# Performance work log

Hardware: AMD Instinct MI355X
Metric: run time of the kernel (lower is better)

## Reference

```python
import jax, jax.numpy as jnp
import numpy as np
from jax import lax

V, E, H, B, T = 50000, 100, 64, 128, 1024


def setup_inputs() -> dict:
    key = jax.random.key(0)
    ks = jax.random.split(key, 16)
    def u(k, shape, fan):
        s = 1.0 / np.sqrt(fan)
        return jax.random.uniform(k, shape, jnp.float32, -s, s)
    x = jax.random.randint(ks[0], (B, T), 0, V)
    emb = jax.random.normal(ks[1], (V, E), jnp.float32)
    emb = emb.at[0].set(0.0)  # padding_idx=0
    return {
        'x': x,
        'emb': emb,
        'Wih0': u(ks[2], (4 * H, E), H), 'Whh0': u(ks[3], (4 * H, H), H),
        'bih0': u(ks[4], (4 * H,), H), 'bhh0': u(ks[5], (4 * H,), H),
        'Wih1': u(ks[6], (4 * H, H), H), 'Whh1': u(ks[7], (4 * H, H), H),
        'bih1': u(ks[8], (4 * H,), H), 'bhh1': u(ks[9], (4 * H,), H),
        'W1': u(ks[10], (H, H), H), 'b1': u(ks[11], (H,), H),
        'W2': u(ks[12], (1, H), H), 'b2': u(ks[13], (1,), H),
    }


def lstm_layer(inp, Wih, Whh, bih, bhh):
    # inp: [B, T, D]; PyTorch gate order i, f, g, o
    b, h = inp.shape[0], Whh.shape[1]
    xw = jnp.einsum('btd,gd->btg', inp, Wih) + bih + bhh  # [B, T, 4H]
    def step(carry, xw_t):
        hs, cs = carry
        gates = xw_t + hs @ Whh.T
        i, f, g, o = jnp.split(gates, 4, axis=-1)
        cs = jax.nn.sigmoid(f) * cs + jax.nn.sigmoid(i) * jnp.tanh(g)
        hs = jax.nn.sigmoid(o) * jnp.tanh(cs)
        return (hs, cs), hs
    init = (jnp.zeros((b, h), inp.dtype), jnp.zeros((b, h), inp.dtype))
    _, out = lax.scan(step, init, jnp.swapaxes(xw, 0, 1))  # [T, B, H]
    return jnp.swapaxes(out, 0, 1)


def reference(x, emb, Wih0, Whh0, bih0, bhh0, Wih1, Whh1, bih1, bhh1, W1, b1, W2, b2):
    e = emb[x]                                  # [B, T, E]
    h0 = lstm_layer(e, Wih0, Whh0, bih0, bhh0)  # [B, T, H]
    h1 = lstm_layer(h0, Wih1, Whh1, bih1, bhh1) # [B, T, H]
    last = h1[:, -1, :]                         # [B, H]
    z = jax.nn.relu(last @ W1.T + b1)           # dropout is identity in eval
    return jax.nn.sigmoid(z @ W2.T + b2)        # [B, 1]
```

## Files before the change

### kernel.cpp

```cpp
#include <hip/hip_runtime.h>
#include <hip/hip_bf16.h>

#define EMB_D 100
#define HID 64
#define G4 256
#define BATCH 128
#define SEQ 1024
#define TOK 64
#define LOG2E 1.44269504f

typedef _Float16 half2v __attribute__((ext_vector_type(2)));
typedef unsigned short u16;
typedef unsigned int   u32;

__device__ __forceinline__ float rcpf(float x) { return __builtin_amdgcn_rcpf(x); }
__device__ __forceinline__ float ex2(float x) { return __builtin_amdgcn_exp2f(x); }
__device__ __forceinline__ float sig_pre(float xp) { return rcpf(1.0f + ex2(-xp)); }
__device__ __forceinline__ float tanh_pre(float xp) {
  float t = ex2(-2.0f * fabsf(xp));
  return copysignf((1.0f - t) * rcpf(1.0f + t), xp);
}
__device__ __forceinline__ float tanh_nat(float x) {
  float t = ex2(-2.885390082f * fabsf(x));
  return copysignf((1.0f - t) * rcpf(1.0f + t), x);
}
__device__ __forceinline__ float sig_nat(float x) { return rcpf(1.0f + ex2(-LOG2E * x)); }

__device__ __forceinline__ float dot2(u32 h, u32 w, float acc) {
  return __builtin_amdgcn_fdot2(__builtin_bit_cast(half2v, h),
                                __builtin_bit_cast(half2v, w), acc, false);
}
__device__ __forceinline__ u32 packh2(float lo, float hi) {
  u16 a = __builtin_bit_cast(u16, (_Float16)lo);
  u16 b = __builtin_bit_cast(u16, (_Float16)hi);
  return (u32)a | ((u32)b << 16);
}
#define QP_XOR1 0xB1
#define QP_XOR2 0x4E
#define QP_XOR3 0x1B
#define QPERM(x, ctrl)                                                        \
  __builtin_bit_cast(float, __builtin_amdgcn_mov_dpp(                         \
      __builtin_bit_cast(int, (x)), (ctrl), 0xF, 0xF, true))

__global__ void prep_kernel(const float* __restrict__ Wih0,
                            const float* __restrict__ Whh0, const float* __restrict__ Wih1,
                            const float* __restrict__ Whh1,
                            const float* __restrict__ bih0, const float* __restrict__ bhh0,
                            const float* __restrict__ bih1, const float* __restrict__ bhh1,
                            u32* __restrict__ Wih0T2, float* __restrict__ b0c,
                            float* __restrict__ b1c,
                            u32* __restrict__ Whh0h, u32* __restrict__ Wih1h,
                            u32* __restrict__ Whh1h) {
  int g = threadIdx.x;
  b0c[g] = (bih0[g] + bhh0[g]) * LOG2E;
  b1c[g] = (bih1[g] + bhh1[g]) * LOG2E;
  for (int dp = 0; dp < 50; ++dp)
    Wih0T2[dp * G4 + g] = packh2(Wih0[g * EMB_D + 2 * dp] * LOG2E,
                                 Wih0[g * EMB_D + 2 * dp + 1] * LOG2E);
  for (int d = 0; d < 32; ++d) {
    Whh0h[g * 32 + d] = packh2(Whh0[g * HID + 2 * d] * LOG2E, Whh0[g * HID + 2 * d + 1] * LOG2E);
    Wih1h[g * 32 + d] = packh2(Wih1[g * HID + 2 * d] * LOG2E, Wih1[g * HID + 2 * d + 1] * LOG2E);
    Whh1h[g * 32 + d] = packh2(Whh1[g * HID + 2 * d] * LOG2E, Whh1[g * HID + 2 * d + 1] * LOG2E);
  }
}

__global__ __attribute__((amdgpu_waves_per_eu(1, 4))) __launch_bounds__(256)
void xw0_kernel(
    const int* __restrict__ x, const float* __restrict__ emb,
    const u32* __restrict__ Wih0T2, const float* __restrict__ b0c,
    _Float16* __restrict__ xw0h) {
  __shared__ int sidx[TOK];
  __shared__ alignas(16) u32 erow[TOK][52];
  int g = threadIdx.x;
  long t0 = (long)blockIdx.x * TOK;

  if (g < TOK) sidx[g] = x[t0 + g];
  __syncthreads();
  for (int i = g; i < TOK * 50; i += 256) {
    int tok = i / 50, dp = i - tok * 50;
    const float* er = emb + (size_t)sidx[tok] * EMB_D + 2 * dp;
    erow[tok][dp] = packh2(er[0], er[1]);
  }
  for (int i = g; i < TOK * 2; i += 256) erow[i >> 1][50 + (i & 1)] = 0;

  u32 wreg[52];
  #pragma unroll
  for (int dp = 0; dp < 50; ++dp) wreg[dp] = Wih0T2[dp * G4 + g];
  wreg[50] = 0; wreg[51] = 0;
  float bb = b0c[g];
  __syncthreads();

  for (int tok = 0; tok < TOK; ++tok) {
    const uint4* ep = (const uint4*)erow[tok];
    float a0 = bb, a1 = 0.f, a2 = 0.f, a3 = 0.f;
    #pragma unroll
    for (int c = 0; c < 13; ++c) {
      uint4 hv = ep[c];
      a0 = dot2(hv.x, wreg[4 * c],     a0);
      a1 = dot2(hv.y, wreg[4 * c + 1], a1);
      a2 = dot2(hv.z, wreg[4 * c + 2], a2);
      a3 = dot2(hv.w, wreg[4 * c + 3], a3);
    }
    xw0h[(t0 + tok) * G4 + g] = (_Float16)((a0 + a1) + (a2 + a3));
  }
}

__global__ __attribute__((amdgpu_waves_per_eu(1, 1))) __launch_bounds__(256)
void lstm_fused_kernel(
    const _Float16* __restrict__ xw0h,
    const u32* __restrict__ Whh0h, const u32* __restrict__ Wih1h,
    const u32* __restrict__ Whh1h, const float* __restrict__ b1c,
    const float* __restrict__ W1, const float* __restrict__ clsb1,
    const float* __restrict__ W2, const float* __restrict__ clsb2,
    float* __restrict__ out) {
  int tid = threadIdx.x;
  int l = tid & 63;
  int w = tid >> 6;
  int e = w * 16 + (l >> 2);
  int k = l & 3;
  int row = k * HID + e;
  int b = blockIdx.x;

  __shared__ alignas(16) _Float16 h0s[2][HID];
  __shared__ alignas(16) _Float16 h1s[2][HID];
  __shared__ alignas(16) float hf[HID];

  uint4 w0[8], w1[8], w2[8];
  {
    const uint4* p0 = (const uint4*)(Whh0h + row * 32);
    const uint4* p1 = (const uint4*)(Wih1h + row * 32);
    const uint4* p2 = (const uint4*)(Whh1h + row * 32);
    #pragma unroll
    for (int c = 0; c < 8; ++c) { w0[c] = p0[c]; w1[c] = p1[c]; w2[c] = p2[c]; }
  }
  #pragma unroll
  for (int c = 0; c < 8; ++c) {
    asm volatile("" : "+v"(w0[c].x), "+v"(w0[c].y), "+v"(w0[c].z), "+v"(w0[c].w));
    asm volatile("" : "+v"(w1[c].x), "+v"(w1[c].y), "+v"(w1[c].z), "+v"(w1[c].w));
    asm volatile("" : "+v"(w2[c].x), "+v"(w2[c].y), "+v"(w2[c].z), "+v"(w2[c].w));
  }
  float bias = b1c[row];

  if (tid < 128) ((u16*)h0s)[tid] = 0;
  else           ((u16*)h1s)[tid - 128] = 0;

  const _Float16* xr = xw0h + (long)b * SEQ * G4 + row;
  float xw_t = (float)xr[0];
  float xw_t1 = (float)xr[G4];
  float c0 = 0.f, c1 = 0.f;
  __syncthreads();

  for (int t = 0; t <= SEQ; ++t) {
    int rb = (t + 1) & 1, wb = t & 1;
    uint4 hc0[8], hc1[8];
    {
      const uint4* p0 = (const uint4*)h0s[rb];
      const uint4* p1 = (const uint4*)h1s[rb];
      #pragma unroll
      for (int c = 0; c < 8; ++c) { hc0[c] = p0[c]; hc1[c] = p1[c]; }
    }
    int tn = (t + 2 < SEQ) ? (t + 2) : (SEQ - 1);
    float xw_t2 = (float)xr[(long)tn * G4];

    if (t < SEQ) {
      float a0 = xw_t, a1 = 0.f, a2 = 0.f, a3 = 0.f;
      #pragma unroll
      for (int c = 0; c < 8; ++c) {
        a0 = dot2(hc0[c].x, w0[c].x, a0);
        a1 = dot2(hc0[c].y, w0[c].y, a1);
        a2 = dot2(hc0[c].z, w0[c].z, a2);
        a3 = dot2(hc0[c].w, w0[c].w, a3);
      }
      float g0 = (a0 + a1) + (a2 + a3);
      float g0x1 = QPERM(g0, QP_XOR1);
      float g0x2 = QPERM(g0, QP_XOR2);
      float g0x3 = QPERM(g0, QP_XOR3);
      c0 = sig_pre(g0x1) * c0 + sig_pre(g0) * tanh_pre(g0x2);
      float hv0 = sig_pre(g0x3) * tanh_nat(c0);
      if (k == 0) h0s[wb][e] = (_Float16)hv0;
    }

    if (t >= 1) {
      float a0 = bias, a1 = 0.f, a2 = 0.f, a3 = 0.f;
      float b0 = 0.f, b1 = 0.f, b2 = 0.f, b3 = 0.f;
      #pragma unroll
      for (int c = 0; c < 8; ++c) {
        a0 = dot2(hc0[c].x, w1[c].x, a0);
        a1 = dot2(hc0[c].y, w1[c].y, a1);
        a2 = dot2(hc0[c].z, w1[c].z, a2);
        a3 = dot2(hc0[c].w, w1[c].w, a3);
        b0 = dot2(hc1[c].x, w2[c].x, b0);
        b1 = dot2(hc1[c].y, w2[c].y, b1);
        b2 = dot2(hc1[c].z, w2[c].z, b2);
        b3 = dot2(hc1[c].w, w2[c].w, b3);
      }
      float g1 = ((a0 + a1) + (a2 + a3)) + ((b0 + b1) + (b2 + b3));
      float g1x1 = QPERM(g1, QP_XOR1);
      float g1x2 = QPERM(g1, QP_XOR2);
      float g1x3 = QPERM(g1, QP_XOR3);
      c1 = sig_pre(g1x1) * c1 + sig_pre(g1) * tanh_pre(g1x2);
      float hv1 = sig_pre(g1x3) * tanh_nat(c1);
      if (k == 0) {
        h1s[wb][e] = (_Float16)hv1;
        if (t == SEQ) hf[e] = hv1;
      }
    }

    xw_t = xw_t1; xw_t1 = xw_t2;
    asm volatile("s_waitcnt lgkmcnt(0)" ::: "memory");
    __builtin_amdgcn_s_barrier();
    asm volatile("" ::: "memory");
  }
  __syncthreads();

  if (w == 0) {
    int j = l;
    const float4* wp = (const float4*)(W1 + j * HID);
    const float4* hp = (const float4*)hf;
    float z0 = clsb1[j], z1 = 0.f, z2 = 0.f, z3 = 0.f;
    #pragma unroll
    for (int c = 0; c < 16; ++c) {
      float4 wv = wp[c];
      float4 hv = hp[c];
      z0 = fmaf(hv.x, wv.x, z0);
      z1 = fmaf(hv.y, wv.y, z1);
      z2 = fmaf(hv.z, wv.z, z2);
      z3 = fmaf(hv.w, wv.w, z3);
    }
    float z = fmaxf((z0 + z1) + (z2 + z3), 0.f);
    float v = z * W2[j];
    v += __shfl_xor(v, 1);
    v += __shfl_xor(v, 2);
    v += __shfl_xor(v, 4);
    v += __shfl_xor(v, 8);
    v += __shfl_xor(v, 16);
    v += __shfl_xor(v, 32);
    if (l == 0) out[b] = sig_nat(v + clsb2[0]);
  }
}

extern "C" void kernel_launch(void* const* d_in, const int* in_sizes, int n_in,
                              void* d_out, int out_size, void* d_ws, size_t ws_size,
                              hipStream_t stream) {
  const int*   x    = (const int*)d_in[0];
  const float* emb  = (const float*)d_in[1];
  const float* Wih0 = (const float*)d_in[2];
  const float* Whh0 = (const float*)d_in[3];
  const float* bih0 = (const float*)d_in[4];
  const float* bhh0 = (const float*)d_in[5];
  const float* Wih1 = (const float*)d_in[6];
  const float* Whh1 = (const float*)d_in[7];
  const float* bih1 = (const float*)d_in[8];
  const float* bhh1 = (const float*)d_in[9];
  const float* W1   = (const float*)d_in[10];
  const float* b1   = (const float*)d_in[11];
  const float* W2   = (const float*)d_in[12];
  const float* b2   = (const float*)d_in[13];
  float* out = (float*)d_out;

  char* ws = (char*)d_ws;
  const size_t XW0_BYTES = (size_t)BATCH * SEQ * G4 * sizeof(_Float16);
  _Float16* xw0h = (_Float16*)ws;     ws += XW0_BYTES;
  u32* Wih0T2    = (u32*)ws;          ws += (size_t)50 * G4 * sizeof(u32);
  float* b0c     = (float*)ws;        ws += G4 * sizeof(float);
  float* b1c     = (float*)ws;        ws += G4 * sizeof(float);
  u32* Whh0h     = (u32*)ws;          ws += (size_t)G4 * 32 * sizeof(u32);
  u32* Wih1h     = (u32*)ws;          ws += (size_t)G4 * 32 * sizeof(u32);
  u32* Whh1h     = (u32*)ws;          ws += (size_t)G4 * 32 * sizeof(u32);

  prep_kernel<<<1, 256, 0, stream>>>(Wih0, Whh0, Wih1, Whh1, bih0, bhh0, bih1, bhh1,
                                     Wih0T2, b0c, b1c, Whh0h, Wih1h, Whh1h);
  xw0_kernel<<<(BATCH * SEQ) / TOK, 256, 0, stream>>>(x, emb, Wih0T2, b0c, xw0h);
  lstm_fused_kernel<<<BATCH, 256, 0, stream>>>(xw0h, Whh0h, Wih1h, Whh1h, b1c,
                                               W1, b1, W2, b2, out);
}
```

Before: 737.6 us.

## Split hidden dot products across quad lanes with DPP reduction instead of gate split

Each quad of lanes previously owned one gate row each and computed the full 64-long dot product, then exchanged gate values via DPP. Now each lane computes a quarter of the K dimension for all four gates of a hidden unit, and the partial sums are reduced across the quad with two DPP adds. The xw0 precompute is rewritten in a gate-interleaved layout so each lane reads all four gate inputs with one 8-byte load. This shortens the per-step LDS read of h (32 bytes per lane instead of 128) and the serial dot2 chain, at the cost of extra DPP reduction steps and a lane-redundant activation computation.

```diff
diff --git a/kernel.cpp b/kernel.cpp
--- a/kernel.cpp
+++ b/kernel.cpp
@@ -35,12 +35,24 @@
   u16 b = __builtin_bit_cast(u16, (_Float16)hi);
   return (u32)a | ((u32)b << 16);
 }
-#define QP_XOR1 0xB1
-#define QP_XOR2 0x4E
-#define QP_XOR3 0x1B
-#define QPERM(x, ctrl)                                                        \
-  __builtin_bit_cast(float, __builtin_amdgcn_mov_dpp(                         \
-      __builtin_bit_cast(int, (x)), (ctrl), 0xF, 0xF, true))
+template <int CTRL>
+__device__ __forceinline__ float dppadd(float v) {
+  int x = __builtin_amdgcn_mov_dpp(__builtin_bit_cast(int, v), CTRL, 0xF, 0xF, true);
+  return v + __builtin_bit_cast(float, x);
+}
+#define QREDUCE(v) do { v = dppadd<0xB1>(v); v = dppadd<0x4E>(v); } while (0)
+
+__device__ __forceinline__ float q8(uint4 ha, uint4 hb, uint4 wa, uint4 wb) {
+  float a0 = dot2(ha.x, wa.x, 0.f);
+  float a1 = dot2(ha.y, wa.y, 0.f);
+  float a2 = dot2(ha.z, wa.z, 0.f);
+  float a3 = dot2(ha.w, wa.w, 0.f);
+  a0 = dot2(hb.x, wb.x, a0);
+  a1 = dot2(hb.y, wb.y, a1);
+  a2 = dot2(hb.z, wb.z, a2);
+  a3 = dot2(hb.w, wb.w, a3);
+  return (a0 + a1) + (a2 + a3);
+}
 
 __global__ void prep_kernel(const float* __restrict__ Wih0,
                             const float* __restrict__ Whh0, const float* __restrict__ Wih1,
@@ -48,12 +60,17 @@
                             const float* __restrict__ bih0, const float* __restrict__ bhh0,
                             const float* __restrict__ bih1, const float* __restrict__ bhh1,
                             u32* __restrict__ Wih0T2, float* __restrict__ b0c,
-                            float* __restrict__ b1c,
+                            float4* __restrict__ b1q,
                             u32* __restrict__ Whh0h, u32* __restrict__ Wih1h,
                             u32* __restrict__ Whh1h) {
   int g = threadIdx.x;
   b0c[g] = (bih0[g] + bhh0[g]) * LOG2E;
-  b1c[g] = (bih1[g] + bhh1[g]) * LOG2E;
+  if (g < HID) {
+    b1q[g] = make_float4((bih1[g] + bhh1[g]) * LOG2E,
+                         (bih1[g + 64] + bhh1[g + 64]) * LOG2E,
+                         (bih1[g + 128] + bhh1[g + 128]) * LOG2E,
+                         (bih1[g + 192] + bhh1[g + 192]) * LOG2E);
+  }
   for (int dp = 0; dp < 50; ++dp)
     Wih0T2[dp * G4 + g] = packh2(Wih0[g * EMB_D + 2 * dp] * LOG2E,
                                  Wih0[g * EMB_D + 2 * dp + 1] * LOG2E);
@@ -68,7 +85,7 @@
 void xw0_kernel(
     const int* __restrict__ x, const float* __restrict__ emb,
     const u32* __restrict__ Wih0T2, const float* __restrict__ b0c,
-    _Float16* __restrict__ xw0h) {
+    u16* __restrict__ xwP) {
   __shared__ int sidx[TOK];
   __shared__ alignas(16) u32 erow[TOK][52];
   int g = threadIdx.x;
@@ -90,6 +107,7 @@
   float bb = b0c[g];
   __syncthreads();
 
+  const int e = g & 63, q = g >> 6;
   for (int tok = 0; tok < TOK; ++tok) {
     const uint4* ep = (const uint4*)erow[tok];
     float a0 = bb, a1 = 0.f, a2 = 0.f, a3 = 0.f;
@@ -101,15 +119,16 @@
       a2 = dot2(hv.z, wreg[4 * c + 2], a2);
       a3 = dot2(hv.w, wreg[4 * c + 3], a3);
     }
-    xw0h[(t0 + tok) * G4 + g] = (_Float16)((a0 + a1) + (a2 + a3));
+    xwP[((size_t)(t0 + tok)) * G4 + e * 4 + q] =
+        __builtin_bit_cast(u16, (_Float16)((a0 + a1) + (a2 + a3)));
   }
 }
 
 __global__ __attribute__((amdgpu_waves_per_eu(1, 1))) __launch_bounds__(256)
 void lstm_fused_kernel(
-    const _Float16* __restrict__ xw0h,
+    const u16* __restrict__ xwP,
     const u32* __restrict__ Whh0h, const u32* __restrict__ Wih1h,
-    const u32* __restrict__ Whh1h, const float* __restrict__ b1c,
+    const u32* __restrict__ Whh1h, const float4* __restrict__ b1q,
     const float* __restrict__ W1, const float* __restrict__ clsb1,
     const float* __restrict__ W2, const float* __restrict__ clsb2,
     float* __restrict__ out) {
@@ -118,7 +137,6 @@
   int w = tid >> 6;
   int e = w * 16 + (l >> 2);
   int k = l & 3;
-  int row = k * HID + e;
   int b = blockIdx.x;
 
   __shared__ alignas(16) _Float16 h0s[2][HID];
@@ -126,12 +144,15 @@
   __shared__ alignas(16) float hf[HID];
 
   uint4 w0[8], w1[8], w2[8];
-  {
-    const uint4* p0 = (const uint4*)(Whh0h + row * 32);
-    const uint4* p1 = (const uint4*)(Wih1h + row * 32);
-    const uint4* p2 = (const uint4*)(Whh1h + row * 32);
-    #pragma unroll
-    for (int c = 0; c < 8; ++c) { w0[c] = p0[c]; w1[c] = p1[c]; w2[c] = p2[c]; }
+  #pragma unroll
+  for (int g = 0; g < 4; ++g) {
+    int row = g * HID + e;
+    const uint4* p0 = (const uint4*)(Whh0h + row * 32 + 8 * k);
+    const uint4* p1 = (const uint4*)(Wih1h + row * 32 + 8 * k);
+    const uint4* p2 = (const uint4*)(Whh1h + row * 32 + 8 * k);
+    w0[2 * g] = p0[0]; w0[2 * g + 1] = p0[1];
+    w1[2 * g] = p1[0]; w1[2 * g + 1] = p1[1];
+    w2[2 * g] = p2[0]; w2[2 * g + 1] = p2[1];
   }
   #pragma unroll
   for (int c = 0; c < 8; ++c) {
@@ -139,74 +160,65 @@
     asm volatile("" : "+v"(w1[c].x), "+v"(w1[c].y), "+v"(w1[c].z), "+v"(w1[c].w));
     asm volatile("" : "+v"(w2[c].x), "+v"(w2[c].y), "+v"(w2[c].z), "+v"(w2[c].w));
   }
-  float bias = b1c[row];
+  float4 bq = b1q[e];
 
   if (tid < 128) ((u16*)h0s)[tid] = 0;
   else           ((u16*)h1s)[tid - 128] = 0;
 
-  const _Float16* xr = xw0h + (long)b * SEQ * G4 + row;
-  float xw_t = (float)xr[0];
-  float xw_t1 = (float)xr[G4];
+  const u16* xb = xwP + (size_t)b * SEQ * G4 + e * 4;
+  uint2 xwA = *(const uint2*)(xb);
+  uint2 xwB = *(const uint2*)(xb + G4);
   float c0 = 0.f, c1 = 0.f;
   __syncthreads();
 
   for (int t = 0; t <= SEQ; ++t) {
     int rb = (t + 1) & 1, wb = t & 1;
-    uint4 hc0[8], hc1[8];
+    uint4 h0a, h0b, h1a, h1b;
     {
       const uint4* p0 = (const uint4*)h0s[rb];
       const uint4* p1 = (const uint4*)h1s[rb];
-      #pragma unroll
-      for (int c = 0; c < 8; ++c) { hc0[c] = p0[c]; hc1[c] = p1[c]; }
+      h0a = p0[2 * k]; h0b = p0[2 * k + 1];
+      h1a = p1[2 * k]; h1b = p1[2 * k + 1];
     }
     int tn = (t + 2 < SEQ) ? (t + 2) : (SEQ - 1);
-    float xw_t2 = (float)xr[(long)tn * G4];
+    uint2 xwC = *(const uint2*)(xb + (size_t)tn * G4);
 
     if (t < SEQ) {
-      float a0 = xw_t, a1 = 0.f, a2 = 0.f, a3 = 0.f;
-      #pragma unroll
-      for (int c = 0; c < 8; ++c) {
-        a0 = dot2(hc0[c].x, w0[c].x, a0);
-        a1 = dot2(hc0[c].y, w0[c].y, a1);
-        a2 = dot2(hc0[c].z, w0[c].z, a2);
-        a3 = dot2(hc0[c].w, w0[c].w, a3);
-      }
-      float g0 = (a0 + a1) + (a2 + a3);
-      float g0x1 = QPERM(g0, QP_XOR1);
-      float g0x2 = QPERM(g0, QP_XOR2);
-      float g0x3 = QPERM(g0, QP_XOR3);
-      c0 = sig_pre(g0x1) * c0 + sig_pre(g0) * tanh_pre(g0x2);
-      float hv0 = sig_pre(g0x3) * tanh_nat(c0);
+      float p0 = q8(h0a, h0b, w0[0], w0[1]);
+      float p1 = q8(h0a, h0b, w0[2], w0[3]);
+      float p2 = q8(h0a, h0b, w0[4], w0[5]);
+      float p3 = q8(h0a, h0b, w0[6], w0[7]);
+      QREDUCE(p0); QREDUCE(p1); QREDUCE(p2); QREDUCE(p3);
+      half2v xif = __builtin_bit_cast(half2v, xwA.x);
+      half2v xgo = __builtin_bit_cast(half2v, xwA.y);
+      float gi = p0 + (float)xif[0];
+      float gf = p1 + (float)xif[1];
+      float gg = p2 + (float)xgo[0];
+      float go = p3 + (float)xgo[1];
+      c0 = sig_pre(gf) * c0 + sig_pre(gi) * tanh_pre(gg);
+      float hv0 = sig_pre(go) * tanh_nat(c0);
       if (k == 0) h0s[wb][e] = (_Float16)hv0;
     }
 
     if (t >= 1) {
-      float a0 = bias, a1 = 0.f, a2 = 0.f, a3 = 0.f;
-      float b0 = 0.f, b1 = 0.f, b2 = 0.f, b3 = 0.f;
-      #pragma unroll
-      for (int c = 0; c < 8; ++c) {
-        a0 = dot2(hc0[c].x, w1[c].x, a0);
-        a1 = dot2(hc0[c].y, w1[c].y, a1);
-        a2 = dot2(hc0[c].z, w1[c].z, a2);
-        a3 = dot2(hc0[c].w, w1[c].w, a3);
-        b0 = dot2(hc1[c].x, w2[c].x, b0);
-        b1 = dot2(hc1[c].y, w2[c].y, b1);
-        b2 = dot2(hc1[c].z, w2[c].z, b2);
-        b3 = dot2(hc1[c].w, w2[c].w, b3);
-      }
-      float g1 = ((a0 + a1) + (a2 + a3)) + ((b0 + b1) + (b2 + b3));
-      float g1x1 = QPERM(g1, QP_XOR1);
-      float g1x2 = QPERM(g1, QP_XOR2);
-      float g1x3 = QPERM(g1, QP_XOR3);
-      c1 = sig_pre(g1x1) * c1 + sig_pre(g1) * tanh_pre(g1x2);
-      float hv1 = sig_pre(g1x3) * tanh_nat(c1);
+      float p0 = q8(h0a, h0b, w1[0], w1[1]) + q8(h1a, h1b, w2[0], w2[1]);
+      float p1 = q8(h0a, h0b, w1[2], w1[3]) + q8(h1a, h1b, w2[2], w2[3]);
+      float p2 = q8(h0a, h0b, w1[4], w1[5]) + q8(h1a, h1b, w2[4], w2[5]);
+      float p3 = q8(h0a, h0b, w1[6], w1[7]) + q8(h1a, h1b, w2[6], w2[7]);
+      QREDUCE(p0); QREDUCE(p1); QREDUCE(p2); QREDUCE(p3);
+      float gi = p0 + bq.x;
+      float gf = p1 + bq.y;
+      float gg = p2 + bq.z;
+      float go = p3 + bq.w;
+      c1 = sig_pre(gf) * c1 + sig_pre(gi) * tanh_pre(gg);
+      float hv1 = sig_pre(go) * tanh_nat(c1);
       if (k == 0) {
         h1s[wb][e] = (_Float16)hv1;
         if (t == SEQ) hf[e] = hv1;
       }
     }
 
-    xw_t = xw_t1; xw_t1 = xw_t2;
+    xwA = xwB; xwB = xwC;
     asm volatile("s_waitcnt lgkmcnt(0)" ::: "memory");
     __builtin_amdgcn_s_barrier();
     asm volatile("" ::: "memory");
@@ -259,18 +271,18 @@
   float* out = (float*)d_out;
 
   char* ws = (char*)d_ws;
-  const size_t XW0_BYTES = (size_t)BATCH * SEQ * G4 * sizeof(_Float16);
-  _Float16* xw0h = (_Float16*)ws;     ws += XW0_BYTES;
-  u32* Wih0T2    = (u32*)ws;          ws += (size_t)50 * G4 * sizeof(u32);
-  float* b0c     = (float*)ws;        ws += G4 * sizeof(float);
-  float* b1c     = (float*)ws;        ws += G4 * sizeof(float);
-  u32* Whh0h     = (u32*)ws;          ws += (size_t)G4 * 32 * sizeof(u32);
-  u32* Wih1h     = (u32*)ws;          ws += (size_t)G4 * 32 * sizeof(u32);
-  u32* Whh1h     = (u32*)ws;          ws += (size_t)G4 * 32 * sizeof(u32);
+  const size_t XW0_BYTES = (size_t)BATCH * SEQ * G4 * sizeof(u16);
+  u16* xwP     = (u16*)ws;       ws += XW0_BYTES;
+  u32* Wih0T2  = (u32*)ws;       ws += (size_t)50 * G4 * sizeof(u32);
+  float* b0c   = (float*)ws;     ws += G4 * sizeof(float);
+  float4* b1q  = (float4*)ws;    ws += (size_t)HID * sizeof(float4);
+  u32* Whh0h   = (u32*)ws;       ws += (size_t)G4 * 32 * sizeof(u32);
+  u32* Wih1h   = (u32*)ws;       ws += (size_t)G4 * 32 * sizeof(u32);
+  u32* Whh1h   = (u32*)ws;       ws += (size_t)G4 * 32 * sizeof(u32);
 
   prep_kernel<<<1, 256, 0, stream>>>(Wih0, Whh0, Wih1, Whh1, bih0, bhh0, bih1, bhh1,
-                                     Wih0T2, b0c, b1c, Whh0h, Wih1h, Whh1h);
-  xw0_kernel<<<(BATCH * SEQ) / TOK, 256, 0, stream>>>(x, emb, Wih0T2, b0c, xw0h);
-  lstm_fused_kernel<<<BATCH, 256, 0, stream>>>(xw0h, Whh0h, Wih1h, Whh1h, b1c,
+                                     Wih0T2, b0c, b1q, Whh0h, Wih1h, Whh1h);
+  xw0_kernel<<<(BATCH * SEQ) / TOK, 256, 0, stream>>>(x, emb, Wih0T2, b0c, xwP);
+  lstm_fused_kernel<<<BATCH, 256, 0, stream>>>(xwP, Whh0h, Wih1h, Whh1h, b1q,
                                                W1, b1, W2, b2, out);
 }
```

Measured after the change: 780.5 us. +5.8%, slower.
